# Kernel optimization log

Measured on AMD Instinct MI355X. Metric: run time of the kernel, lower is better.

The kernel has to match this reference:

```python
import jax, jax.numpy as jnp
import numpy as np

# Model config (mirrors init_kwargs)
N_HEADS = 32
N_KV_HEADS = 8
HEAD_DIM = 128
DIM = 4096
FREQ_BASE = 500000.0
MAX_SEQ_LEN = 8192
B = 16
T = 16


def _ggml_rope(x, pos):
    """ggml-style RoPE (mode 0): rotates adjacent pairs (x[2i], x[2i+1]).
    x: [B, T, H, HEAD_DIM], pos: [T] int."""
    half = HEAD_DIM // 2
    inv_freq = FREQ_BASE ** (-(jnp.arange(half, dtype=jnp.float32) * 2.0) / HEAD_DIM)  # [half]
    ang = pos.astype(jnp.float32)[:, None] * inv_freq[None, :]                        # [T, half]
    cos = jnp.cos(ang)[None, :, None, :]  # [1, T, 1, half]
    sin = jnp.sin(ang)[None, :, None, :]
    xr = x.reshape(*x.shape[:-1], half, 2)
    x0, x1 = xr[..., 0], xr[..., 1]
    o0 = x0 * cos - x1 * sin
    o1 = x0 * sin + x1 * cos
    return jnp.stack([o0, o1], axis=-1).reshape(x.shape)


def setup_inputs() -> dict:
    key = jax.random.key(0)
    ks = jax.random.split(key, 10)
    x = jax.random.normal(ks[0], (B, T, DIM), dtype=jnp.float32)
    # decode step at the end of the cache -> kv_len == MAX_SEQ_LEN (static)
    input_pos = jnp.arange(MAX_SEQ_LEN - T, MAX_SEQ_LEN, dtype=jnp.int32)
    # causal mask over the full cache: query i may attend to positions <= input_pos[i]
    js = jnp.arange(MAX_SEQ_LEN)
    attn_mask = jnp.where(js[None, :] <= input_pos[:, None], 0.0, -jnp.inf).astype(jnp.float32)  # [T, kv_len]
    k_cache = jax.random.normal(ks[1], (B, MAX_SEQ_LEN, N_KV_HEADS, HEAD_DIM), dtype=jnp.float32)
    v_cache = jax.random.normal(ks[2], (B, MAX_SEQ_LEN, N_KV_HEADS, HEAD_DIM), dtype=jnp.float32)
    s = 1.0 / np.sqrt(DIM)
    wq = jax.random.normal(ks[3], (N_HEADS * HEAD_DIM, DIM), dtype=jnp.float32) * s
    wk = jax.random.normal(ks[4], (N_KV_HEADS * HEAD_DIM, DIM), dtype=jnp.float32) * s
    wv = jax.random.normal(ks[5], (N_KV_HEADS * HEAD_DIM, DIM), dtype=jnp.float32) * s
    wo = jax.random.normal(ks[6], (DIM, N_HEADS * HEAD_DIM), dtype=jnp.float32) * s
    # freqs_cos/freqs_sin are in the torch forward signature but unused (ggml.rope
    # recomputes them from input_pos + freq_base); kept as dummy inputs.
    half = HEAD_DIM // 2
    freqs_cos = jax.random.uniform(ks[7], (T, half), dtype=jnp.float32)
    freqs_sin = jax.random.uniform(ks[8], (T, half), dtype=jnp.float32)
    return {"x": x, "freqs_cos": freqs_cos, "freqs_sin": freqs_sin,
            "input_pos": input_pos, "attn_mask": attn_mask,
            "k_cache": k_cache, "v_cache": v_cache,
            "wq": wq, "wk": wk, "wv": wv, "wo": wo}


def reference(x, freqs_cos, freqs_sin, input_pos, attn_mask, k_cache, v_cache, wq, wk, wv, wo):
    Bx, Tx, _ = x.shape
    n_rep = N_HEADS // N_KV_HEADS
    q = jnp.einsum('btd,ed->bte', x, wq).reshape(Bx, Tx, N_HEADS, HEAD_DIM)
    k = jnp.einsum('btd,ed->bte', x, wk).reshape(Bx, Tx, N_KV_HEADS, HEAD_DIM)
    v = jnp.einsum('btd,ed->bte', x, wv).reshape(Bx, Tx, N_KV_HEADS, HEAD_DIM)
    q = _ggml_rope(q, input_pos)
    k = _ggml_rope(k, input_pos)
    # KV-cache index_copy along time axis
    k_cache = k_cache.at[:, input_pos].set(k)
    v_cache = v_cache.at[:, input_pos].set(v)
    # kv_len = input_pos[0] + T == MAX_SEQ_LEN here (static), so use full cache.
    kq = k_cache  # [B, S, Hkv, D]
    vq = v_cache
    scale = 1.0 / np.sqrt(HEAD_DIM)
    # GQA: group q heads as [g=n_kv, r=n_rep]; equivalent to repeat_interleave on K/V
    qg = q.reshape(Bx, Tx, N_KV_HEADS, n_rep, HEAD_DIM)
    scores = jnp.einsum('btgrd,bsgd->bgrts', qg, kq) * scale  # [B, g, r, T, S]
    scores = scores + attn_mask  # [T, S] broadcasts
    attn = jax.nn.softmax(scores, axis=-1)
    y = jnp.einsum('bgrts,bsgd->btgrd', attn, vq).reshape(Bx, Tx, N_HEADS * HEAD_DIM)
    return jnp.einsum('bte,de->btd', y, wo)
```

## Files before the change

### kernel.cpp

```cpp
#include <hip/hip_runtime.h>
#include <math.h>

#define SEQ 8192
#define NEWBASE 8176
#define NS 4

typedef short s16x4 __attribute__((ext_vector_type(4)));
typedef short s16x8 __attribute__((ext_vector_type(8)));
typedef float f32x4 __attribute__((ext_vector_type(4)));

__device__ __forceinline__ short f2bf(float f) {
  unsigned u = __float_as_uint(f);
  u += 0x7FFFu + ((u >> 16) & 1u);
  return (short)(u >> 16);
}

__device__ __forceinline__ f32x4 mfma16(s16x8 a, s16x8 b, f32x4 c) {
  return __builtin_amdgcn_mfma_f32_16x16x32_bf16(a, b, c, 0, 0, 0);
}

__device__ __forceinline__ void sync_nodrain() {
  __builtin_amdgcn_sched_barrier(0);
  asm volatile("s_waitcnt lgkmcnt(0)" ::: "memory");
  __builtin_amdgcn_s_barrier();
  __builtin_amdgcn_sched_barrier(0);
}

template<int KSTEPS>
__device__ __forceinline__
void gemm_tile(const float* __restrict__ A, const float* __restrict__ Bw,
               float* __restrict__ Cp, int ldc) {
  __shared__ short As[64 * 72];
  __shared__ short Bs[128 * 72];
  const int tid = threadIdx.x, lane = tid & 63, w = tid >> 6;
  const int l15 = lane & 15, l4 = lane >> 4;
  f32x4 acc[8] = {};
  float4 ar[4], br[8];

  auto issue = [&](int st) {
    const float* Ab = A + st * 64;
    const float* Bb = Bw + st * 64;
#pragma unroll
    for (int i = 0; i < 4; ++i) {
      int id = tid + i * 256;
      ar[i] = *(const float4*)(Ab + (size_t)(id >> 4) * 4096 + ((id & 15) << 2));
    }
#pragma unroll
    for (int i = 0; i < 8; ++i) {
      int id = tid + i * 256;
      br[i] = *(const float4*)(Bb + (size_t)(id >> 4) * 4096 + ((id & 15) << 2));
    }
  };

  issue(0);
  for (int st = 0; st < KSTEPS; ++st) {
#pragma unroll
    for (int i = 0; i < 4; ++i) {
      int id = tid + i * 256, row = id >> 4, c4 = (id & 15) << 2;
      s16x4 h = { f2bf(ar[i].x), f2bf(ar[i].y), f2bf(ar[i].z), f2bf(ar[i].w) };
      *(s16x4*)&As[row * 72 + c4] = h;
    }
#pragma unroll
    for (int i = 0; i < 8; ++i) {
      int id = tid + i * 256, row = id >> 4, c4 = (id & 15) << 2;
      s16x4 h = { f2bf(br[i].x), f2bf(br[i].y), f2bf(br[i].z), f2bf(br[i].w) };
      *(s16x4*)&Bs[row * 72 + c4] = h;
    }
    sync_nodrain();
    if (st + 1 < KSTEPS) issue(st + 1);
    __builtin_amdgcn_sched_barrier(0);
#pragma unroll
    for (int kk = 0; kk < 64; kk += 32) {
      s16x8 a = *(const s16x8*)&As[(w * 16 + l15) * 72 + kk + l4 * 8];
#pragma unroll
      for (int nf = 0; nf < 8; ++nf) {
        s16x8 b = *(const s16x8*)&Bs[(nf * 16 + l15) * 72 + kk + l4 * 8];
        acc[nf] = mfma16(a, b, acc[nf]);
      }
    }
    sync_nodrain();
  }
#pragma unroll
  for (int nf = 0; nf < 8; ++nf)
#pragma unroll
    for (int r = 0; r < 4; ++r)
      Cp[(size_t)(w * 16 + l4 * 4 + r) * ldc + nf * 16 + l15] = acc[nf][r];
}

__global__ __launch_bounds__(256)
__attribute__((amdgpu_waves_per_eu(4, 4)))
void gemm_qkv(const float* __restrict__ x,
              const float* __restrict__ wq, const float* __restrict__ wk,
              const float* __restrict__ wv, float* __restrict__ part,
              const int* __restrict__ ipos,
              float* __restrict__ ctab, float* __restrict__ stab) {
  int bn = blockIdx.x, bm = blockIdx.y, sp = blockIdx.z;
  if (bn == 0 && bm == 0 && sp == 0) {
#pragma unroll
    for (int k = 0; k < 4; ++k) {
      int i = threadIdx.x + k * 256;
      int t = i >> 6, f = i & 63;
      double inv = exp(-((double)(2 * f) / 128.0) * log(500000.0));
      double ang = (double)ipos[t] * inv;
      ctab[i] = (float)cos(ang);
      stab[i] = (float)sin(ang);
    }
  }
  const float* Bw;
  if (bn < 32)      Bw = wq + (size_t)(bn * 128) * 4096;
  else if (bn < 40) Bw = wk + (size_t)((bn - 32) * 128) * 4096;
  else              Bw = wv + (size_t)((bn - 40) * 128) * 4096;
  const float* A = x + (size_t)(bm * 64) * 4096 + sp * 1024;
  float* Cp = part + (size_t)sp * (256 * 6144) + (size_t)(bm * 64) * 6144 + bn * 128;
  gemm_tile<16>(A, Bw + sp * 1024, Cp, 6144);
}

__global__ __launch_bounds__(256)
__attribute__((amdgpu_waves_per_eu(4, 4)))
void gemm_out(const float* __restrict__ y, const float* __restrict__ wo,
              float* __restrict__ part) {
  int bn = blockIdx.x, bm = blockIdx.y, sp = blockIdx.z;
  const float* A = y + (size_t)(bm * 64) * 4096 + sp * 1024;
  const float* Bw = wo + (size_t)(bn * 128) * 4096 + sp * 1024;
  float* Cp = part + (size_t)sp * (256 * 4096) + (size_t)(bm * 64) * 4096 + bn * 128;
  gemm_tile<16>(A, Bw, Cp, 4096);
}

__global__ __launch_bounds__(256)
void rope_reduce(const float* __restrict__ part, const float* __restrict__ ctab,
                 const float* __restrict__ stab, float* __restrict__ q,
                 float* __restrict__ kn, float* __restrict__ vn) {
  int idx = blockIdx.x * 256 + threadIdx.x;
  int m = idx / 3072;
  int col = (idx - m * 3072) * 2;
  const float* src = part + (size_t)m * 6144 + col;
  float a0 = 0.f, a1 = 0.f;
#pragma unroll
  for (int s = 0; s < 4; ++s) {
    a0 += src[(size_t)s * 1572864];
    a1 += src[(size_t)s * 1572864 + 1];
  }
  if (col < 5120) {
    int local = (col < 4096) ? col : col - 4096;
    int f = (local & 127) >> 1, t = m & 15;
    float c = ctab[t * 64 + f], sn = stab[t * 64 + f];
    float o0 = a0 * c - a1 * sn, o1 = a0 * sn + a1 * c;
    if (col < 4096) {
      q[(size_t)m * 4096 + col] = o0;
      q[(size_t)m * 4096 + col + 1] = o1;
    } else {
      kn[(size_t)m * 1024 + local] = o0;
      kn[(size_t)m * 1024 + local + 1] = o1;
    }
  } else {
    int local = col - 5120;
    vn[(size_t)m * 1024 + local] = a0;
    vn[(size_t)m * 1024 + local + 1] = a1;
  }
}

__global__ __launch_bounds__(512)
__attribute__((amdgpu_waves_per_eu(4, 4)))
void attn7(const float* __restrict__ kc_, const float* __restrict__ vc_,
           const float* __restrict__ qb, const float* __restrict__ kn,
           const float* __restrict__ vn, const int* __restrict__ ipos,
           float* __restrict__ pO, float* __restrict__ pL) {
  __shared__ short Ks[2][32 * 128];
  __shared__ short Vt[2][128 * 34];
  __shared__ short Ps[4 * 16 * 40];
  const int sh = blockIdx.x, g = blockIdx.y, b = blockIdx.z;
  const int tid = threadIdx.x, lane = tid & 63, w = tid >> 6;
  const int l15 = lane & 15, l4 = lane >> 4;
  const float scale = 0.08838834764831845f;
  const int sbase = sh * 2048;

  const float* kc_b = kc_ + (size_t)b * SEQ * 1024 + g * 128;
  const float* vc_b = vc_ + (size_t)b * SEQ * 1024 + g * 128;
  const float* kn_b = kn + (size_t)b * 16 * 1024 + g * 128;
  const float* vn_b = vn + (size_t)b * 16 * 1024 + g * 128;

  if (w < 4) {
    const int krow = tid >> 5, kc4 = (tid & 31) << 2;
    const int vcol = tid & 127, vhr = (tid >> 7) << 4;
    float4 kA[4], kB[4];
    float vA[16], vB[16];

    auto issue = [&](int cb, float4 (&kr)[4], float (&vr)[16]) {
      if (cb + 32 <= NEWBASE) {
#pragma unroll
        for (int i = 0; i < 4; ++i)
          kr[i] = *(const float4*)(kc_b + (size_t)(cb + krow + i * 8) * 1024 + kc4);
#pragma unroll
        for (int j = 0; j < 16; ++j)
          vr[j] = vc_b[(size_t)(cb + vhr + j) * 1024 + vcol];
      } else {
#pragma unroll
        for (int i = 0; i < 4; ++i) {
          int sg = cb + krow + i * 8;
          const float* src = (sg >= NEWBASE)
              ? (kn_b + (size_t)(sg - NEWBASE) * 1024 + kc4)
              : (kc_b + (size_t)sg * 1024 + kc4);
          kr[i] = *(const float4*)src;
        }
#pragma unroll
        for (int j = 0; j < 16; ++j) {
          int sg = cb + vhr + j;
          vr[j] = (sg >= NEWBASE)
              ? vn_b[(size_t)(sg - NEWBASE) * 1024 + vcol]
              : vc_b[(size_t)sg * 1024 + vcol];
        }
      }
    };
    auto convert = [&](int buf, const float4 (&kr)[4], const float (&vr)[16]) {
#pragma unroll
      for (int i = 0; i < 4; ++i) {
        int s = krow + i * 8;
        s16x4 hv = { f2bf(kr[i].x), f2bf(kr[i].y), f2bf(kr[i].z), f2bf(kr[i].w) };
        *(s16x4*)&Ks[buf][s * 128 + (kc4 ^ ((s & 7) << 3))] = hv;
      }
#pragma unroll
      for (int j4 = 0; j4 < 4; ++j4) {
        s16x4 hv = { f2bf(vr[j4 * 4]), f2bf(vr[j4 * 4 + 1]),
                     f2bf(vr[j4 * 4 + 2]), f2bf(vr[j4 * 4 + 3]) };
        *(s16x4*)&Vt[buf][vcol * 34 + vhr + j4 * 4] = hv;
      }
    };

    issue(sbase, kA, vA);
    issue(sbase + 32, kB, vB);
    convert(0, kA, vA);
    sync_nodrain();
    for (int c = 1; c < 64; c += 2) {
      convert(1, kB, vB);
      if (c + 1 < 64) issue(sbase + (c + 1) * 32, kA, vA);
      sync_nodrain();
      if (c + 1 < 64) convert(0, kA, vA);
      if (c + 2 < 64) issue(sbase + (c + 2) * 32, kB, vB);
      sync_nodrain();
    }
  } else {
    const int qg = w - 4;
    s16x8 qa[4];
    {
      int qr = qg * 16 + l15;
      int t = qr >> 2, r = qr & 3, h = g * 4 + r;
      const float* qp = qb + (size_t)(b * 16 + t) * 4096 + h * 128;
#pragma unroll
      for (int ks = 0; ks < 4; ++ks) {
        float4 v0 = *(const float4*)(qp + ks * 32 + l4 * 8);
        float4 v1 = *(const float4*)(qp + ks * 32 + l4 * 8 + 4);
        qa[ks] = s16x8{ f2bf(v0.x), f2bf(v0.y), f2bf(v0.z), f2bf(v0.w),
                        f2bf(v1.x), f2bf(v1.y), f2bf(v1.z), f2bf(v1.w) };
      }
    }
    const int ip_t = ipos[qg * 4 + l4];
    f32x4 o[8] = {};
    float lsum[4] = { 0.f, 0.f, 0.f, 0.f };
    short* Pw = &Ps[qg * (16 * 40)];

    sync_nodrain();
    for (int c = 0; c < 64; ++c) {
      const short* Kb = &Ks[c & 1][0];
      const short* Vb = &Vt[c & 1][0];
      const int base = sbase + c * 32;
      f32x4 sc[2] = {};
#pragma unroll
      for (int ks = 0; ks < 4; ++ks) {
        int dd = ks * 32 + l4 * 8;
#pragma unroll
        for (int nf = 0; nf < 2; ++nf) {
          int s = nf * 16 + l15;
          s16x8 kb = *(const s16x8*)&Kb[s * 128 + (dd ^ ((s & 7) << 3))];
          sc[nf] = mfma16(qa[ks], kb, sc[nf]);
        }
      }
#pragma unroll
      for (int nf = 0; nf < 2; ++nf) {
        int sg = base + nf * 16 + l15;
#pragma unroll
        for (int r = 0; r < 4; ++r) {
          float p = (sg <= ip_t) ? __expf(sc[nf][r] * scale) : 0.f;
          lsum[r] += p;
          Pw[(l4 * 4 + r) * 40 + nf * 16 + l15] = f2bf(p);
        }
      }
      s16x8 pa = *(const s16x8*)&Pw[l15 * 40 + l4 * 8];
#pragma unroll
      for (int nd = 0; nd < 8; ++nd) {
        int d = nd * 16 + l15;
        s16x8 vb = *(const s16x8*)&Vb[d * 34 + l4 * 8];
        o[nd] = mfma16(pa, vb, o[nd]);
      }
      sync_nodrain();
    }
#pragma unroll
    for (int r = 0; r < 4; ++r) {
      lsum[r] += __shfl_xor(lsum[r], 1, 64);
      lsum[r] += __shfl_xor(lsum[r], 2, 64);
      lsum[r] += __shfl_xor(lsum[r], 4, 64);
      lsum[r] += __shfl_xor(lsum[r], 8, 64);
    }
    const int blk = (b * 8 + g) * NS + sh;
    float* Ob = pO + (size_t)blk * 64 * 128;
#pragma unroll
    for (int nd = 0; nd < 8; ++nd)
#pragma unroll
      for (int r = 0; r < 4; ++r)
        Ob[(qg * 16 + l4 * 4 + r) * 128 + nd * 16 + l15] = o[nd][r];
    if (l15 == 0) {
#pragma unroll
      for (int r = 0; r < 4; ++r)
        pL[blk * 64 + qg * 16 + l4 * 4 + r] = lsum[r];
    }
  }
}

__global__ __launch_bounds__(256)
void merge(const float* __restrict__ pO, const float* __restrict__ pL,
           float* __restrict__ y) {
  const int gq = blockIdx.x, b = blockIdx.y;
  const int g = gq >> 2, qc = gq & 3;
  const int bb = (b * 8 + g) * NS;
#pragma unroll
  for (int i = 0; i < 8; ++i) {
    int id = qc * 2048 + i * 256 + threadIdx.x;
    int qr = id >> 7, d = id & 127;
    float acc = 0.f, den = 0.f;
#pragma unroll
    for (int p = 0; p < NS; ++p) {
      acc += pO[(size_t)(bb + p) * 8192 + id];
      den += pL[(bb + p) * 64 + qr];
    }
    int t = qr >> 2, r = qr & 3, h = g * 4 + r;
    y[(size_t)(b * 16 + t) * 4096 + h * 128 + d] = acc / den;
  }
}

__global__ __launch_bounds__(256)
void out_reduce(const float* __restrict__ part, float* __restrict__ out) {
  int i = blockIdx.x * 256 + threadIdx.x;
  const f32x4* p4 = (const f32x4*)part;
  f32x4 s = {0.f, 0.f, 0.f, 0.f};
#pragma unroll
  for (int sp = 0; sp < 4; ++sp) s += p4[(size_t)sp * 262144 + i];
  ((f32x4*)out)[i] = s;
}

extern "C" void kernel_launch(void* const* d_in, const int* in_sizes, int n_in,
                              void* d_out, int out_size, void* d_ws, size_t ws_size,
                              hipStream_t stream) {
  const float* x      = (const float*)d_in[0];
  const int*   ipos   = (const int*)d_in[3];
  const float* kcache = (const float*)d_in[5];
  const float* vcache = (const float*)d_in[6];
  const float* wq     = (const float*)d_in[7];
  const float* wk     = (const float*)d_in[8];
  const float* wv     = (const float*)d_in[9];
  const float* wo     = (const float*)d_in[10];
  float* out = (float*)d_out;

  float* q_buf = (float*)d_ws;
  float* k_new = q_buf + 1048576;
  float* v_new = k_new + 262144;
  float* y_buf = v_new + 262144;
  float* ctab  = y_buf + 1048576;
  float* stab  = ctab + 1024;
  float* pO    = stab + 1024;
  float* pL    = pO + 8388608;
  float* qkvp  = pO;
  float* outp  = pO;

  gemm_qkv<<<dim3(48, 4, 4), 256, 0, stream>>>(x, wq, wk, wv, qkvp,
                                               ipos, ctab, stab);
  rope_reduce<<<3072, 256, 0, stream>>>(qkvp, ctab, stab, q_buf, k_new, v_new);
  attn7<<<dim3(NS, 8, 16), 512, 0, stream>>>(kcache, vcache, q_buf, k_new, v_new,
                                             ipos, pO, pL);
  merge<<<dim3(32, 16), 256, 0, stream>>>(pO, pL, y_buf);
  gemm_out<<<dim3(32, 4, 4), 256, 0, stream>>>(y_buf, wo, outp);
  out_reduce<<<1024, 256, 0, stream>>>(outp, out);
}
```

Before: 306.5 us.

## Warp-specialize projection GEMMs into producer and consumer waves with double-buffered LDS

The shared GEMM tile routine now runs with 512 threads: four waves load fp32 tiles from global memory, convert them to bf16 and write them into a double-buffered LDS tile, while four other waves run the MFMA loop and write results. Matched barriers hand each buffer from producers to consumers. The aim is to overlap global loads and conversion with matrix math instead of serialising them within the same waves. It doubles LDS use and raises register pressure in the producer waves, which hold two stages of loads.

```diff
diff --git a/kernel.cpp b/kernel.cpp
--- a/kernel.cpp
+++ b/kernel.cpp
@@ -26,68 +26,85 @@
   __builtin_amdgcn_sched_barrier(0);
 }
 
-template<int KSTEPS>
+template<int KS>
 __device__ __forceinline__
-void gemm_tile(const float* __restrict__ A, const float* __restrict__ Bw,
-               float* __restrict__ Cp, int ldc) {
-  __shared__ short As[64 * 72];
-  __shared__ short Bs[128 * 72];
+void gemm_tile_pc(const float* __restrict__ A, const float* __restrict__ Bw,
+                  float* __restrict__ Cp, int ldc) {
+  __shared__ short As[2][64 * 72];
+  __shared__ short Bs[2][128 * 72];
   const int tid = threadIdx.x, lane = tid & 63, w = tid >> 6;
   const int l15 = lane & 15, l4 = lane >> 4;
-  f32x4 acc[8] = {};
-  float4 ar[4], br[8];
-
-  auto issue = [&](int st) {
-    const float* Ab = A + st * 64;
-    const float* Bb = Bw + st * 64;
-#pragma unroll
-    for (int i = 0; i < 4; ++i) {
-      int id = tid + i * 256;
-      ar[i] = *(const float4*)(Ab + (size_t)(id >> 4) * 4096 + ((id & 15) << 2));
-    }
-#pragma unroll
-    for (int i = 0; i < 8; ++i) {
-      int id = tid + i * 256;
-      br[i] = *(const float4*)(Bb + (size_t)(id >> 4) * 4096 + ((id & 15) << 2));
-    }
-  };
-
-  issue(0);
-  for (int st = 0; st < KSTEPS; ++st) {
-#pragma unroll
-    for (int i = 0; i < 4; ++i) {
-      int id = tid + i * 256, row = id >> 4, c4 = (id & 15) << 2;
-      s16x4 h = { f2bf(ar[i].x), f2bf(ar[i].y), f2bf(ar[i].z), f2bf(ar[i].w) };
-      *(s16x4*)&As[row * 72 + c4] = h;
-    }
-#pragma unroll
-    for (int i = 0; i < 8; ++i) {
-      int id = tid + i * 256, row = id >> 4, c4 = (id & 15) << 2;
-      s16x4 h = { f2bf(br[i].x), f2bf(br[i].y), f2bf(br[i].z), f2bf(br[i].w) };
-      *(s16x4*)&Bs[row * 72 + c4] = h;
-    }
+
+  if (w < 4) {
+    float4 aA[4], aB[4], bA[8], bB[8];
+    auto issue = [&](int st, float4 (&ar)[4], float4 (&br)[8]) {
+      const float* Ab = A + st * 64;
+      const float* Bb = Bw + st * 64;
+#pragma unroll
+      for (int i = 0; i < 4; ++i) {
+        int id = tid + i * 256;
+        ar[i] = *(const float4*)(Ab + (size_t)(id >> 4) * 4096 + ((id & 15) << 2));
+      }
+#pragma unroll
+      for (int i = 0; i < 8; ++i) {
+        int id = tid + i * 256;
+        br[i] = *(const float4*)(Bb + (size_t)(id >> 4) * 4096 + ((id & 15) << 2));
+      }
+    };
+    auto convert = [&](int buf, const float4 (&ar)[4], const float4 (&br)[8]) {
+#pragma unroll
+      for (int i = 0; i < 4; ++i) {
+        int id = tid + i * 256, row = id >> 4, c4 = (id & 15) << 2;
+        s16x4 h = { f2bf(ar[i].x), f2bf(ar[i].y), f2bf(ar[i].z), f2bf(ar[i].w) };
+        *(s16x4*)&As[buf][row * 72 + c4] = h;
+      }
+#pragma unroll
+      for (int i = 0; i < 8; ++i) {
+        int id = tid + i * 256, row = id >> 4, c4 = (id & 15) << 2;
+        s16x4 h = { f2bf(br[i].x), f2bf(br[i].y), f2bf(br[i].z), f2bf(br[i].w) };
+        *(s16x4*)&Bs[buf][row * 72 + c4] = h;
+      }
+    };
+
+    issue(0, aA, bA);
+    issue(1, aB, bB);
+    convert(0, aA, bA);
     sync_nodrain();
-    if (st + 1 < KSTEPS) issue(st + 1);
-    __builtin_amdgcn_sched_barrier(0);
-#pragma unroll
-    for (int kk = 0; kk < 64; kk += 32) {
-      s16x8 a = *(const s16x8*)&As[(w * 16 + l15) * 72 + kk + l4 * 8];
-#pragma unroll
-      for (int nf = 0; nf < 8; ++nf) {
-        s16x8 b = *(const s16x8*)&Bs[(nf * 16 + l15) * 72 + kk + l4 * 8];
-        acc[nf] = mfma16(a, b, acc[nf]);
-      }
-    }
+    for (int c = 1; c < KS; c += 2) {
+      convert(1, aB, bB);
+      if (c + 1 < KS) issue(c + 1, aA, bA);
+      sync_nodrain();
+      if (c + 1 < KS) convert(0, aA, bA);
+      if (c + 2 < KS) issue(c + 2, aB, bB);
+      sync_nodrain();
+    }
+  } else {
+    const int cw = w - 4;
+    f32x4 acc[8] = {};
     sync_nodrain();
-  }
-#pragma unroll
-  for (int nf = 0; nf < 8; ++nf)
-#pragma unroll
-    for (int r = 0; r < 4; ++r)
-      Cp[(size_t)(w * 16 + l4 * 4 + r) * ldc + nf * 16 + l15] = acc[nf][r];
-}
-
-__global__ __launch_bounds__(256)
+    for (int c = 0; c < KS; ++c) {
+      const short* Ab = &As[c & 1][0];
+      const short* Bb = &Bs[c & 1][0];
+#pragma unroll
+      for (int kk = 0; kk < 64; kk += 32) {
+        s16x8 a = *(const s16x8*)&Ab[(cw * 16 + l15) * 72 + kk + l4 * 8];
+#pragma unroll
+        for (int nf = 0; nf < 8; ++nf) {
+          s16x8 b = *(const s16x8*)&Bb[(nf * 16 + l15) * 72 + kk + l4 * 8];
+          acc[nf] = mfma16(a, b, acc[nf]);
+        }
+      }
+      sync_nodrain();
+    }
+#pragma unroll
+    for (int nf = 0; nf < 8; ++nf)
+#pragma unroll
+      for (int r = 0; r < 4; ++r)
+        Cp[(size_t)(cw * 16 + l4 * 4 + r) * ldc + nf * 16 + l15] = acc[nf][r];
+  }
+}
+
+__global__ __launch_bounds__(512)
 __attribute__((amdgpu_waves_per_eu(4, 4)))
 void gemm_qkv(const float* __restrict__ x,
               const float* __restrict__ wq, const float* __restrict__ wk,
@@ -97,8 +114,8 @@
   int bn = blockIdx.x, bm = blockIdx.y, sp = blockIdx.z;
   if (bn == 0 && bm == 0 && sp == 0) {
 #pragma unroll
-    for (int k = 0; k < 4; ++k) {
-      int i = threadIdx.x + k * 256;
+    for (int k = 0; k < 2; ++k) {
+      int i = threadIdx.x + k * 512;
       int t = i >> 6, f = i & 63;
       double inv = exp(-((double)(2 * f) / 128.0) * log(500000.0));
       double ang = (double)ipos[t] * inv;
@@ -112,10 +129,10 @@
   else              Bw = wv + (size_t)((bn - 40) * 128) * 4096;
   const float* A = x + (size_t)(bm * 64) * 4096 + sp * 1024;
   float* Cp = part + (size_t)sp * (256 * 6144) + (size_t)(bm * 64) * 6144 + bn * 128;
-  gemm_tile<16>(A, Bw + sp * 1024, Cp, 6144);
-}
-
-__global__ __launch_bounds__(256)
+  gemm_tile_pc<16>(A, Bw + sp * 1024, Cp, 6144);
+}
+
+__global__ __launch_bounds__(512)
 __attribute__((amdgpu_waves_per_eu(4, 4)))
 void gemm_out(const float* __restrict__ y, const float* __restrict__ wo,
               float* __restrict__ part) {
@@ -123,7 +140,7 @@
   const float* A = y + (size_t)(bm * 64) * 4096 + sp * 1024;
   const float* Bw = wo + (size_t)(bn * 128) * 4096 + sp * 1024;
   float* Cp = part + (size_t)sp * (256 * 4096) + (size_t)(bm * 64) * 4096 + bn * 128;
-  gemm_tile<16>(A, Bw, Cp, 4096);
+  gemm_tile_pc<16>(A, Bw, Cp, 4096);
 }
 
 __global__ __launch_bounds__(256)
@@ -370,12 +387,12 @@
   float* qkvp  = pO;
   float* outp  = pO;
 
-  gemm_qkv<<<dim3(48, 4, 4), 256, 0, stream>>>(x, wq, wk, wv, qkvp,
+  gemm_qkv<<<dim3(48, 4, 4), 512, 0, stream>>>(x, wq, wk, wv, qkvp,
                                                ipos, ctab, stab);
   rope_reduce<<<3072, 256, 0, stream>>>(qkvp, ctab, stab, q_buf, k_new, v_new);
   attn7<<<dim3(NS, 8, 16), 512, 0, stream>>>(kcache, vcache, q_buf, k_new, v_new,
                                              ipos, pO, pL);
   merge<<<dim3(32, 16), 256, 0, stream>>>(pO, pL, y_buf);
-  gemm_out<<<dim3(32, 4, 4), 256, 0, stream>>>(y_buf, wo, outp);
+  gemm_out<<<dim3(32, 4, 4), 512, 0, stream>>>(y_buf, wo, outp);
   out_reduce<<<1024, 256, 0, stream>>>(outp, out);
 }
```

After: 293.3 us. -4.3%, faster.
